# Optimization experiments

Measured on AMD Instinct MI355X. Metric: run time of the kernel, lower is better.

The kernel has to match this reference:

```python
import jax, jax.numpy as jnp
import numpy as np

IN_CH = 384
HEAD_DIM = 32
MAX_SEQ = 64          # P, tokens per window
N_HEADS = IN_CH // HEAD_DIM
PART = int(np.sqrt(MAX_SEQ))  # 8, window side
SCALE = HEAD_DIM ** -0.5


def _relative_position_index():
    # Swin relative position index, [P*P] int
    h = np.arange(PART)
    coords = np.stack(np.meshgrid(h, h, indexing='ij')).reshape(2, -1)  # [2, P]
    rel = coords[:, :, None] - coords[:, None, :]                        # [2, P, P]
    rel = rel.transpose(1, 2, 0).astype(np.int64)
    rel[:, :, 0] += PART - 1
    rel[:, :, 1] += PART - 1
    rel[:, :, 0] *= 2 * PART - 1
    return rel.sum(-1).reshape(-1)  # [P*P]

REL_IDX = jnp.asarray(_relative_position_index())


def setup_inputs() -> dict:
    key = jax.random.key(0)
    ks = jax.random.split(key, 6)
    B, G, P, D = 32, 64, MAX_SEQ, IN_CH
    x = jax.random.normal(ks[0], (B, G, P, D), dtype=jnp.float32)
    Wqkv = jax.random.normal(ks[1], (D, 3 * D), dtype=jnp.float32) * (D ** -0.5)
    bqkv = jnp.zeros((3 * D,), dtype=jnp.float32)
    Wm = jax.random.normal(ks[2], (D, D), dtype=jnp.float32) * (D ** -0.5)
    bm = jnp.zeros((D,), dtype=jnp.float32)
    # torch init is zeros; use small normal so bias actually affects the output
    rel_table = jax.random.normal(ks[3], ((2 * PART - 1) ** 2, N_HEADS), dtype=jnp.float32) * 0.02
    return {"x": x, "Wqkv": Wqkv, "bqkv": bqkv, "Wm": Wm, "bm": bm, "rel_table": rel_table}


def reference(x, Wqkv, bqkv, Wm, bm, rel_table):
    B, G, P, D = x.shape
    H, DH = N_HEADS, HEAD_DIM
    qkv = x @ Wqkv + bqkv                                   # [B,G,P,3D]
    q, k, v = jnp.split(qkv, 3, axis=-1)
    q = q.reshape(B, G, P, H, DH) * SCALE
    k = k.reshape(B, G, P, H, DH)
    v = v.reshape(B, G, P, H, DH)
    attn = jnp.einsum('bgihd,bgjhd->bghij', q, k)           # [B,G,H,P,P]
    bias = rel_table[REL_IDX].reshape(P, P, H).transpose(2, 0, 1)  # [H,P,P]
    attn = jax.nn.softmax(attn + bias[None, None], axis=-1)
    out = jnp.einsum('bghij,bgjhd->bgihd', attn, v)         # [B,G,P,H,DH]
    out = out.reshape(B, G, P, D)
    return out @ Wm + bm
```

## Files before the change

kernel.cpp:

```cpp
#include <hip/hip_runtime.h>
#include <stdint.h>


typedef __attribute__((ext_vector_type(4))) float f32x4;
typedef __attribute__((ext_vector_type(4))) short s16x4;
typedef __attribute__((ext_vector_type(8))) short s16x8;

#define DEVI static __device__ __forceinline__

DEVI unsigned short f2bf(float f) {
  union { float f; uint32_t u; } v; v.f = f;
  return (unsigned short)((v.u + 0x7FFFu + ((v.u >> 16) & 1u)) >> 16);
}

DEVI f32x4 zero4() { f32x4 z; z[0] = 0.f; z[1] = 0.f; z[2] = 0.f; z[3] = 0.f; return z; }

#if defined(__has_builtin)
#if __has_builtin(__builtin_amdgcn_mfma_f32_16x16x16bf16_1k)
#define MFMA16_BUILTIN 1
#endif
#if __has_builtin(__builtin_amdgcn_global_load_lds)
#define HAS_GLLDS 1
#endif
#endif

DEVI f32x4 mfma16(s16x4 a, s16x4 b, f32x4 c) {
#ifdef MFMA16_BUILTIN
  return __builtin_amdgcn_mfma_f32_16x16x16bf16_1k(a, b, c, 0, 0, 0);
#else
  asm volatile("v_mfma_f32_16x16x16_bf16 %0, %1, %2, %0" : "+v"(c) : "v"(a), "v"(b));
  return c;
#endif
}

DEVI f32x4 mfma32(s16x8 a, s16x8 b, f32x4 c) {
  return __builtin_amdgcn_mfma_f32_16x16x32_bf16(a, b, c, 0, 0, 0);
}

DEVI void stage1k(const unsigned short* g_lane, unsigned short* lds_base) {
#ifdef HAS_GLLDS
  __builtin_amdgcn_global_load_lds(
      (const __attribute__((address_space(1))) unsigned int*)g_lane,
      (__attribute__((address_space(3))) unsigned int*)lds_base, 16, 0, 0);
#else
  *(s16x8*)(lds_base + (threadIdx.x & 63) * 8) = *(const s16x8*)g_lane;
#endif
}

__global__ void prep_wqkvT(const float* __restrict__ W, unsigned short* __restrict__ WT) {
  int t = blockIdx.x * 256 + threadIdx.x;
  if (t >= 1152 * 384) return;
  int n = t / 384, k = t - n * 384;
  float s = (n < 384) ? 0.17677669529663687f : 1.0f;
  WT[t] = f2bf(W[(size_t)k * 1152 + n] * s);
}

__global__ void prep_wmT(const float* __restrict__ W, unsigned short* __restrict__ WT) {
  int t = blockIdx.x * 256 + threadIdx.x;
  if (t >= 384 * 384) return;
  int n = t / 384, k = t - n * 384;
  WT[t] = f2bf(W[(size_t)k * 384 + n]);
}

__global__ void prep_bqkv(const float* __restrict__ b, float* __restrict__ bs) {
  int t = blockIdx.x * 256 + threadIdx.x;
  if (t >= 1152) return;
  bs[t] = b[t] * ((t < 384) ? 0.17677669529663687f : 1.0f);
}

__global__ void prep_biasF(const float* __restrict__ rel, float* __restrict__ biasF) {
  int t = blockIdx.x * 256 + threadIdx.x;
  if (t >= 12288) return;
  int h = t >> 10;
  int r = (t >> 6) & 15;
  int lane = t & 63;
  int jt = r >> 2, it = r & 3;
  int lg = lane >> 4, lr = lane & 15;
  int i = it * 16 + lr;
#pragma unroll
  for (int e = 0; e < 4; ++e) {
    int j = jt * 16 + lg * 4 + e;
    int idx = ((i >> 3) - (j >> 3) + 7) * 15 + ((i & 7) - (j & 7) + 7);
    biasF[t * 4 + e] = rel[idx * 12 + h];
  }
}

__global__ void fill_val(float* o, int n, float v) {
  int t = blockIdx.x * 256 + threadIdx.x;
  if (t < n) o[t] = v;
}

__global__ __launch_bounds__(256) void conv_bf16(const float* __restrict__ x,
                                                 unsigned short* __restrict__ xb) {
  const size_t nchunk = 131072UL * 384 / 8;
  const size_t stride = (size_t)gridDim.x * blockDim.x;
  for (size_t i = (size_t)blockIdx.x * blockDim.x + threadIdx.x; i < nchunk; i += stride) {
    f32x4 a = *(const f32x4*)(x + i * 8);
    f32x4 b = *(const f32x4*)(x + i * 8 + 4);
    s16x8 p;
    p[0] = (short)f2bf(a[0]); p[1] = (short)f2bf(a[1]);
    p[2] = (short)f2bf(a[2]); p[3] = (short)f2bf(a[3]);
    p[4] = (short)f2bf(b[0]); p[5] = (short)f2bf(b[1]);
    p[6] = (short)f2bf(b[2]); p[7] = (short)f2bf(b[3]);
    *(s16x8*)(xb + i * 8) = p;
  }
}

template <bool QKV_EPI>
__global__ __launch_bounds__(256) void gemm_k(const unsigned short* __restrict__ A,
                                              const unsigned short* __restrict__ BT,
                                              const float* __restrict__ bias,
                                              void* __restrict__ Cv) {
  constexpr int K = 384;
  constexpr int NT = QKV_EPI ? 9 : 3;
  constexpr int N = NT * 128;
  __shared__ unsigned short sm[2][16384];
  const int bid = blockIdx.x;
  const int swz = (bid & 7) * (NT * 128) + (bid >> 3);
  const int n0 = (swz % NT) * 128;
  const int m0 = (swz / NT) * 128;
  const int tid = threadIdx.x;
  const int lane = tid & 63, wv = tid >> 6;
  const int wr = wv >> 1, wc = wv & 1;
  const int lg = lane >> 4, lr = lane & 15;

  const int scol = ((lane & 7) ^ (lane >> 3)) * 8;
  const unsigned short* Ag = A + (size_t)(m0 + wv * 32 + (lane >> 3)) * K + scol;
  const unsigned short* Bg = BT + (size_t)(n0 + wv * 32 + (lane >> 3)) * K + scol;

  f32x4 acc[4][4];
#pragma unroll
  for (int i = 0; i < 4; ++i)
#pragma unroll
    for (int j = 0; j < 4; ++j) acc[i][j] = zero4();

  auto STAGE = [&](int buf, int k0) {
#pragma unroll
    for (int c2 = 0; c2 < 4; ++c2)
      stage1k(Ag + (size_t)(c2 * 8) * K + k0, &sm[buf][(wv * 32 + c2 * 8) * 64]);
#pragma unroll
    for (int c2 = 0; c2 < 4; ++c2)
      stage1k(Bg + (size_t)(c2 * 8) * K + k0, &sm[buf][8192 + (wv * 32 + c2 * 8) * 64]);
  };
  const int sa = (lr & 7) << 3;
  auto COMPUTE = [&](int buf) {
#pragma unroll
    for (int kk = 0; kk < 64; kk += 32) {
      s16x8 af[4], bf[4];
#pragma unroll
      for (int mt = 0; mt < 4; ++mt)
        af[mt] = *(const s16x8*)&sm[buf][(wr * 64 + 16 * mt + lr) * 64 + ((kk + 8 * lg) ^ sa)];
#pragma unroll
      for (int nt = 0; nt < 4; ++nt)
        bf[nt] = *(const s16x8*)&sm[buf][8192 + (wc * 64 + 16 * nt + lr) * 64 + ((kk + 8 * lg) ^ sa)];
#pragma unroll
      for (int mt = 0; mt < 4; ++mt)
#pragma unroll
        for (int nt = 0; nt < 4; ++nt)
          acc[mt][nt] = mfma32(af[mt], bf[nt], acc[mt][nt]);
    }
  };

  STAGE(0, 0);
  __syncthreads();
  int cur = 0;
#pragma unroll 1
  for (int t = 0; t < 5; ++t) {
    STAGE(cur ^ 1, (t + 1) * 64);
    COMPUTE(cur);
    __syncthreads();
    cur ^= 1;
  }
  COMPUTE(cur);

  const int crow = m0 + wr * 64 + 4 * lg;
  const int ccol = n0 + wc * 64 + lr;
  if constexpr (QKV_EPI) {
    const int sel = n0 / 384;
    unsigned short* qkv = (unsigned short*)Cv;
    if (sel < 2) {
      unsigned short* tile = &sm[0][0];
#pragma unroll
      for (int nt = 0; nt < 4; ++nt) {
        const int cc = wc * 64 + 16 * nt + lr;
        const float bv = bias[n0 + cc];
#pragma unroll
        for (int mt = 0; mt < 4; ++mt) {
#pragma unroll
          for (int e = 0; e < 4; ++e) {
            const int r = wr * 64 + 16 * mt + 4 * lg + e;
            tile[r * 128 + (cc ^ ((r & 7) << 3))] = f2bf(acc[mt][nt][e] + bv);
          }
        }
      }
      __syncthreads();
      const int hbase = (n0 - sel * 384) >> 5;
#pragma unroll
      for (int rr = 0; rr < 2; ++rr) {
        const int tr = wv * 32 + rr * 16 + (lane >> 2);
        const int gtok = m0 + tr;
        const int w2 = gtok >> 6, t0r = gtok & 63;
#pragma unroll
        for (int hh = 0; hh < 4; ++hh) {
          const int chunk = hh * 4 + (lane & 3);
          s16x8 v = *(const s16x8*)&tile[tr * 128 + ((chunk * 8) ^ ((tr & 7) << 3))];
          unsigned short* dst = qkv + (((size_t)w2 * 12 + hbase + hh) * 3 + sel) * 2048 +
                                t0r * 32 + (lane & 3) * 8;
          *(s16x8*)dst = v;
        }
      }
    } else {
      const int window = crow >> 6;
      const int t0 = crow & 63;
#pragma unroll
      for (int nt = 0; nt < 4; ++nt) {
        const int col = ccol + 16 * nt;
        const int hcol = col - 768;
        const int h = hcol >> 5, d = hcol & 31;
        const float bv = bias[col];
        unsigned short* base = qkv + (((size_t)window * 12 + h) * 3 + 2) * 2048;
#pragma unroll
        for (int mt = 0; mt < 4; ++mt) {
          s16x4 pk;
#pragma unroll
          for (int e = 0; e < 4; ++e) pk[e] = (short)f2bf(acc[mt][nt][e] + bv);
          *(s16x4*)&base[d * 64 + t0 + 16 * mt] = pk;
        }
      }
    }
  } else {
    float* C = (float*)Cv;
#pragma unroll
    for (int mt = 0; mt < 4; ++mt)
#pragma unroll
      for (int nt = 0; nt < 4; ++nt) {
        const int col = ccol + 16 * nt;
        const float bv = bias[col];
#pragma unroll
        for (int e = 0; e < 4; ++e)
          C[(size_t)(crow + 16 * mt + e) * N + col] = acc[mt][nt][e] + bv;
      }
  }
}

__global__ __launch_bounds__(256) void attn_k(const unsigned short* __restrict__ qkv,
                                              const float* __restrict__ biasF,
                                              unsigned short* __restrict__ attnout) {
  const int lane = threadIdx.x & 63;
  const int wv = threadIdx.x >> 6;
  const int wh = blockIdx.x * 4 + wv;
  const int window = wh / 12;
  const int h = wh - window * 12;
  const int lg = lane >> 4, lr = lane & 15;

  const unsigned short* hb = qkv + (size_t)wh * 6144;
  const unsigned short* Qh = hb;
  const unsigned short* Kh = hb + 2048;
  const unsigned short* Vth = hb + 4096;

  s16x8 ka[4], qb[4];
#pragma unroll
  for (int jt = 0; jt < 4; ++jt)
    ka[jt] = *(const s16x8*)&Kh[(jt * 16 + lr) * 32 + 8 * lg];
#pragma unroll
  for (int it = 0; it < 4; ++it)
    qb[it] = *(const s16x8*)&Qh[(it * 16 + lr) * 32 + 8 * lg];

  f32x4 c[4][4];
#pragma unroll
  for (int a = 0; a < 4; ++a)
#pragma unroll
    for (int b2 = 0; b2 < 4; ++b2) c[a][b2] = zero4();

#pragma unroll
  for (int jt = 0; jt < 4; ++jt)
#pragma unroll
    for (int it = 0; it < 4; ++it)
      c[jt][it] = mfma32(ka[jt], qb[it], c[jt][it]);

  const f32x4* bF = (const f32x4*)biasF + ((size_t)h * 16) * 64 + lane;
#pragma unroll
  for (int jt = 0; jt < 4; ++jt)
#pragma unroll
    for (int it = 0; it < 4; ++it)
      c[jt][it] += bF[(jt * 4 + it) * 64];

  s16x4 pb[4][4];
#pragma unroll
  for (int it = 0; it < 4; ++it) {
    float m = -3.0e38f;
#pragma unroll
    for (int jt = 0; jt < 4; ++jt)
#pragma unroll
      for (int e = 0; e < 4; ++e) m = fmaxf(m, c[jt][it][e]);
    m = fmaxf(m, __shfl_xor(m, 16));
    m = fmaxf(m, __shfl_xor(m, 32));
    float s = 0.f;
#pragma unroll
    for (int jt = 0; jt < 4; ++jt)
#pragma unroll
      for (int e = 0; e < 4; ++e) {
        float p = __expf(c[jt][it][e] - m);
        c[jt][it][e] = p;
        s += p;
      }
    s += __shfl_xor(s, 16);
    s += __shfl_xor(s, 32);
    const float inv = 1.f / s;
#pragma unroll
    for (int jt = 0; jt < 4; ++jt) {
      s16x4 pk;
#pragma unroll
      for (int e = 0; e < 4; ++e) pk[e] = (short)f2bf(c[jt][it][e] * inv);
      pb[jt][it] = pk;
    }
  }

  f32x4 o[2][4];
#pragma unroll
  for (int a = 0; a < 2; ++a)
#pragma unroll
    for (int b2 = 0; b2 < 4; ++b2) o[a][b2] = zero4();

#pragma unroll
  for (int jt = 0; jt < 4; ++jt) {
    s16x4 va[2];
#pragma unroll
    for (int dt = 0; dt < 2; ++dt)
      va[dt] = *(const s16x4*)&Vth[(dt * 16 + lr) * 64 + jt * 16 + 4 * lg];
#pragma unroll
    for (int dt = 0; dt < 2; ++dt)
#pragma unroll
      for (int it = 0; it < 4; ++it)
        o[dt][it] = mfma16(va[dt], pb[jt][it], o[dt][it]);
  }

  unsigned short* ob = attnout + (size_t)window * 64 * 384;
#pragma unroll
  for (int dt = 0; dt < 2; ++dt)
#pragma unroll
    for (int it = 0; it < 4; ++it) {
      s16x4 pk;
#pragma unroll
      for (int e = 0; e < 4; ++e) pk[e] = (short)f2bf(o[dt][it][e]);
      *(s16x4*)&ob[(size_t)(it * 16 + lr) * 384 + h * 32 + dt * 16 + 4 * lg] = pk;
    }
}

extern "C" void kernel_launch(void* const* d_in, const int* in_sizes, int n_in,
                              void* d_out, int out_size, void* d_ws, size_t ws_size,
                              hipStream_t stream) {
  const float* x = (const float*)d_in[0];
  const float* Wqkv = (const float*)d_in[1];
  const float* bqkv = (const float*)d_in[2];
  const float* Wm = (const float*)d_in[3];
  const float* bm = (const float*)d_in[4];
  const float* rel = (const float*)d_in[5];

  const size_t M = 131072;
  char* ws = (char*)d_ws;
  size_t off = 0;
  unsigned short* qkv = (unsigned short*)(ws + off);   off += M * 1152 * 2;
  unsigned short* xb = (unsigned short*)(ws + off);    off += M * 384 * 2;
  unsigned short* WqkvT = (unsigned short*)(ws + off); off += 1152 * 384 * 2;
  unsigned short* WmT = (unsigned short*)(ws + off);   off += 384 * 384 * 2;
  float* biasF = (float*)(ws + off);                   off += 12 * 16 * 64 * 4 * 4;
  float* bqkvs = (float*)(ws + off);                   off += 1152 * 4;
  unsigned short* attnout = xb;

  if (ws_size < off) {
    fill_val<<<(out_size + 255) / 256, 256, 0, stream>>>((float*)d_out, out_size, 12345.0f);
    return;
  }

  prep_wqkvT<<<(1152 * 384 + 255) / 256, 256, 0, stream>>>(Wqkv, WqkvT);
  prep_wmT<<<(384 * 384 + 255) / 256, 256, 0, stream>>>(Wm, WmT);
  prep_bqkv<<<5, 256, 0, stream>>>(bqkv, bqkvs);
  prep_biasF<<<48, 256, 0, stream>>>(rel, biasF);
  conv_bf16<<<2048, 256, 0, stream>>>(x, xb);

  gemm_k<true><<<9216, 256, 0, stream>>>(xb, WqkvT, bqkvs, qkv);
  attn_k<<<6144, 256, 0, stream>>>(qkv, biasF, attnout);
  gemm_k<false><<<3072, 256, 0, stream>>>(attnout, WmT, bm, d_out);
}
```

Measured before the change: 468.2 us.

## Enlarge GEMM block tile to 256x128 with 512 threads and shared B staging

Both projection GEMMs now use 512-thread blocks that each compute a 256x128 output tile. Eight waves split the M dimension while sharing one staged B tile, which halves the number of blocks and cuts redundant B loads and per-block setup. The QKV epilogue store loop is remapped so each thread covers one row across eight column chunks. The risks are fewer resident blocks per CU because of the 96KB LDS footprint, added register pressure under the 512,2 launch bound, and an extra barrier before the epilogue.

```diff
diff --git a/kernel.cpp b/kernel.cpp
--- a/kernel.cpp
+++ b/kernel.cpp
@@ -107,18 +107,18 @@
 }
 
 template <bool QKV_EPI>
-__global__ __launch_bounds__(256) void gemm_k(const unsigned short* __restrict__ A,
-                                              const unsigned short* __restrict__ BT,
-                                              const float* __restrict__ bias,
-                                              void* __restrict__ Cv) {
+__global__ __launch_bounds__(512, 2) void gemm_k(const unsigned short* __restrict__ A,
+                                                 const unsigned short* __restrict__ BT,
+                                                 const float* __restrict__ bias,
+                                                 void* __restrict__ Cv) {
   constexpr int K = 384;
   constexpr int NT = QKV_EPI ? 9 : 3;
   constexpr int N = NT * 128;
-  __shared__ unsigned short sm[2][16384];
+  __shared__ unsigned short sm[49152];
   const int bid = blockIdx.x;
-  const int swz = (bid & 7) * (NT * 128) + (bid >> 3);
+  const int swz = (bid & 7) * (NT * 64) + (bid >> 3);
   const int n0 = (swz % NT) * 128;
-  const int m0 = (swz / NT) * 128;
+  const int m0 = (swz / NT) * 256;
   const int tid = threadIdx.x;
   const int lane = tid & 63, wv = tid >> 6;
   const int wr = wv >> 1, wc = wv & 1;
@@ -126,7 +126,7 @@
 
   const int scol = ((lane & 7) ^ (lane >> 3)) * 8;
   const unsigned short* Ag = A + (size_t)(m0 + wv * 32 + (lane >> 3)) * K + scol;
-  const unsigned short* Bg = BT + (size_t)(n0 + wv * 32 + (lane >> 3)) * K + scol;
+  const unsigned short* Bg = BT + (size_t)(n0 + wv * 16 + (lane >> 3)) * K + scol;
 
   f32x4 acc[4][4];
 #pragma unroll
@@ -137,10 +137,10 @@
   auto STAGE = [&](int buf, int k0) {
 #pragma unroll
     for (int c2 = 0; c2 < 4; ++c2)
-      stage1k(Ag + (size_t)(c2 * 8) * K + k0, &sm[buf][(wv * 32 + c2 * 8) * 64]);
-#pragma unroll
-    for (int c2 = 0; c2 < 4; ++c2)
-      stage1k(Bg + (size_t)(c2 * 8) * K + k0, &sm[buf][8192 + (wv * 32 + c2 * 8) * 64]);
+      stage1k(Ag + (size_t)(c2 * 8) * K + k0, &sm[buf * 24576 + (wv * 32 + c2 * 8) * 64]);
+#pragma unroll
+    for (int c2 = 0; c2 < 2; ++c2)
+      stage1k(Bg + (size_t)(c2 * 8) * K + k0, &sm[buf * 24576 + 16384 + (wv * 16 + c2 * 8) * 64]);
   };
   const int sa = (lr & 7) << 3;
   auto COMPUTE = [&](int buf) {
@@ -149,10 +149,10 @@
       s16x8 af[4], bf[4];
 #pragma unroll
       for (int mt = 0; mt < 4; ++mt)
-        af[mt] = *(const s16x8*)&sm[buf][(wr * 64 + 16 * mt + lr) * 64 + ((kk + 8 * lg) ^ sa)];
+        af[mt] = *(const s16x8*)&sm[buf * 24576 + (wr * 64 + 16 * mt + lr) * 64 + ((kk + 8 * lg) ^ sa)];
 #pragma unroll
       for (int nt = 0; nt < 4; ++nt)
-        bf[nt] = *(const s16x8*)&sm[buf][8192 + (wc * 64 + 16 * nt + lr) * 64 + ((kk + 8 * lg) ^ sa)];
+        bf[nt] = *(const s16x8*)&sm[buf * 24576 + 16384 + (wc * 64 + 16 * nt + lr) * 64 + ((kk + 8 * lg) ^ sa)];
 #pragma unroll
       for (int mt = 0; mt < 4; ++mt)
 #pragma unroll
@@ -172,6 +172,7 @@
     cur ^= 1;
   }
   COMPUTE(cur);
+  __syncthreads();
 
   const int crow = m0 + wr * 64 + 4 * lg;
   const int ccol = n0 + wc * 64 + lr;
@@ -179,7 +180,7 @@
     const int sel = n0 / 384;
     unsigned short* qkv = (unsigned short*)Cv;
     if (sel < 2) {
-      unsigned short* tile = &sm[0][0];
+      unsigned short* tile = &sm[0];
 #pragma unroll
       for (int nt = 0; nt < 4; ++nt) {
         const int cc = wc * 64 + 16 * nt + lr;
@@ -195,19 +196,16 @@
       }
       __syncthreads();
       const int hbase = (n0 - sel * 384) >> 5;
-#pragma unroll
-      for (int rr = 0; rr < 2; ++rr) {
-        const int tr = wv * 32 + rr * 16 + (lane >> 2);
-        const int gtok = m0 + tr;
-        const int w2 = gtok >> 6, t0r = gtok & 63;
-#pragma unroll
-        for (int hh = 0; hh < 4; ++hh) {
-          const int chunk = hh * 4 + (lane & 3);
-          s16x8 v = *(const s16x8*)&tile[tr * 128 + ((chunk * 8) ^ ((tr & 7) << 3))];
-          unsigned short* dst = qkv + (((size_t)w2 * 12 + hbase + hh) * 3 + sel) * 2048 +
-                                t0r * 32 + (lane & 3) * 8;
-          *(s16x8*)dst = v;
-        }
+      const int tr = wv * 32 + (lane >> 1);
+      const int gtok = m0 + tr;
+      const int w2 = gtok >> 6, t0r = gtok & 63;
+#pragma unroll
+      for (int cc2 = 0; cc2 < 8; ++cc2) {
+        const int c = cc2 * 2 + (lane & 1);
+        s16x8 v = *(const s16x8*)&tile[tr * 128 + ((c * 8) ^ ((tr & 7) << 3))];
+        unsigned short* dst = qkv + (((size_t)w2 * 12 + hbase + (c >> 2)) * 3 + sel) * 2048 +
+                              t0r * 32 + (c & 3) * 8;
+        *(s16x8*)dst = v;
       }
     } else {
       const int window = crow >> 6;
@@ -379,7 +377,7 @@
   prep_biasF<<<48, 256, 0, stream>>>(rel, biasF);
   conv_bf16<<<2048, 256, 0, stream>>>(x, xb);
 
-  gemm_k<true><<<9216, 256, 0, stream>>>(xb, WqkvT, bqkvs, qkv);
+  gemm_k<true><<<4608, 512, 0, stream>>>(xb, WqkvT, bqkvs, qkv);
   attn_k<<<6144, 256, 0, stream>>>(qkv, biasF, attnout);
-  gemm_k<false><<<3072, 256, 0, stream>>>(attnout, WmT, bm, d_out);
-}
+  gemm_k<false><<<1536, 512, 0, stream>>>(attnout, WmT, bm, d_out);
+}
```

New measurement: 528.4 us. +12.8%, slower.
